# Kernel optimization log

Measured on AMD Instinct MI355X. Metric: run time of the kernel, lower is better.

Reference implementation:

```python
import jax, jax.numpy as jnp
import numpy as np

T, B, E, H = 2048, 4, 1024, 16
D = E // H  # head_dim = 64
SCALING = D ** -0.5


def setup_inputs() -> dict:
    key = jax.random.key(0)
    ks = jax.random.split(key, 5)
    w_scale = (2.0 / (E + E)) ** 0.5  # xavier_uniform-ish std
    return {
        "query": jax.random.normal(ks[0], (T, B, E), dtype=jnp.float32),
        "q_weight": jax.random.normal(ks[1], (E, E), dtype=jnp.float32) * w_scale,
        "k_weight": jax.random.normal(ks[2], (E, E), dtype=jnp.float32) * w_scale,
        "v_weight": jax.random.normal(ks[3], (E, E), dtype=jnp.float32) * w_scale,
        "out_proj_weight": jax.random.normal(ks[4], (E, E), dtype=jnp.float32) * w_scale,
        "q_bias": jnp.zeros((E,), dtype=jnp.float32),
        "k_bias": jnp.zeros((E,), dtype=jnp.float32),
        "v_bias": jnp.zeros((E,), dtype=jnp.float32),
        "out_proj_bias": jnp.zeros((E,), dtype=jnp.float32),
    }


def reference(query, q_weight, k_weight, v_weight, out_proj_weight,
              q_bias, k_bias, v_bias, out_proj_bias):
    # Linear projections: y = x @ W.T + b  (torch F.linear convention)
    q = jnp.einsum('tbe,fe->tbf', query, q_weight) + q_bias
    k = jnp.einsum('tbe,fe->tbf', query, k_weight) + k_bias
    v = jnp.einsum('tbe,fe->tbf', query, v_weight) + v_bias
    # split heads: [T, B, H, D]
    q = q.reshape(T, B, H, D) * SCALING
    k = k.reshape(T, B, H, D)
    v = v.reshape(T, B, H, D)
    # attention scores [B, H, T, T] over keys s
    scores = jnp.einsum('tbhd,sbhd->bhts', q, k)
    attn = jax.nn.softmax(scores, axis=-1)
    # context [T, B, H, D] -> [T, B, E]
    ctx = jnp.einsum('bhts,sbhd->tbhd', attn, v).reshape(T, B, E)
    # output projection
    out = jnp.einsum('tbe,fe->tbf', ctx, out_proj_weight) + out_proj_bias
    return out
```

## Files before the change

kernel.cpp:

```cpp
#include <hip/hip_runtime.h>
#include <hip/hip_bf16.h>
#include <stdint.h>

#define T_   2048
#define B_   4
#define E_   1024
#define H_   16
#define D_   64
#define M_   8192
#define KDIM 1024

using bf16 = __hip_bfloat16;
typedef __attribute__((ext_vector_type(8)))  short bf16x8;
typedef __attribute__((ext_vector_type(4)))  float f32x4;
typedef __attribute__((ext_vector_type(16))) float f32x16;

#define QK_SCALE 0.180336880f

#if __has_builtin(__builtin_amdgcn_exp2f)
#define EXP2F(x) __builtin_amdgcn_exp2f(x)
#else
#define EXP2F(x) exp2f(x)
#endif

__device__ __forceinline__ void gload_lds16(const void* g, void* l) {
  __builtin_amdgcn_global_load_lds(
      (const __attribute__((address_space(1))) void*)g,
      (__attribute__((address_space(3))) void*)l, 16, 0, 0);
}

__device__ __forceinline__ uint32_t pack_bf16(float lo, float hi) {
  union { __hip_bfloat162 h2; uint32_t u; } cv;
  cv.h2 = __float22bfloat162_rn(float2{lo, hi});
  return cv.u;
}

__device__ __forceinline__ void plswap(uint32_t& a, uint32_t& b) {
#if __has_builtin(__builtin_amdgcn_permlane32_swap)
  typedef __attribute__((ext_vector_type(2))) unsigned int u32x2_t;
  u32x2_t r = __builtin_amdgcn_permlane32_swap(a, b, false, false);
  a = r[0]; b = r[1];
#else
  asm volatile("v_permlane32_swap_b32 %0, %1" : "+v"(a), "+v"(b));
#endif
}
__device__ __forceinline__ float comb_add32(float x) {
  union { float f; uint32_t u; } a, b; a.f = x; b.f = x;
  plswap(a.u, b.u);
  return a.f + b.f;
}

__global__ void k_cvt_all(const float* __restrict__ X,
                          const float* __restrict__ Wq, const float* __restrict__ Wk,
                          const float* __restrict__ Wv, const float* __restrict__ Wo,
                          bf16* __restrict__ Xb,
                          bf16* __restrict__ Wqb, bf16* __restrict__ Wkb,
                          bf16* __restrict__ Wvb, bf16* __restrict__ Wob) {
  int id = blockIdx.x;
  const float* src; bf16* dst; int base;
  if (id < 8192) { src = X; dst = Xb; base = id; }
  else {
    int w = (id - 8192) >> 10;
    base = (id - 8192) & 1023;
    src = (w == 0) ? Wq : (w == 1) ? Wk : (w == 2) ? Wv : Wo;
    dst = (w == 0) ? Wqb : (w == 1) ? Wkb : (w == 2) ? Wvb : Wob;
  }
  int i = base * 256 + threadIdx.x;
  float4 v = reinterpret_cast<const float4*>(src)[i];
  bf16* d = dst + (size_t)i * 4;
  d[0] = __float2bfloat16(v.x);
  d[1] = __float2bfloat16(v.y);
  d[2] = __float2bfloat16(v.z);
  d[3] = __float2bfloat16(v.w);
}

__device__ __forceinline__ void gemm_tile_body(
    const bf16* __restrict__ A, const bf16* __restrict__ Bw,
    int bm, int bn, bf16* sA, bf16* sB, f32x4 (&acc)[4][4])
{
  const int t    = threadIdx.x;
  const int wave = t >> 6;
  const int lane = t & 63;
  const int l15  = lane & 15, l4 = lane >> 4;
  const int wr = wave >> 1, wc = wave & 1;
  const int srow = t >> 3;
  const int sg   = t & 7;

  for (int k0 = 0; k0 < KDIM; k0 += 64) {
#pragma unroll
    for (int rd = 0; rd < 4; ++rd) {
      int row = rd * 32 + srow;
      const bf16* src = A + (size_t)(bm * 128 + row) * KDIM + k0 + ((sg ^ (row & 7)) * 8);
      gload_lds16(src, sA + rd * 2048 + wave * 512);
    }
#pragma unroll
    for (int rd = 0; rd < 4; ++rd) {
      int row = rd * 32 + srow;
      const bf16* src = Bw + (size_t)(bn * 128 + row) * KDIM + k0 + ((sg ^ (row & 7)) * 8);
      gload_lds16(src, sB + rd * 2048 + wave * 512);
    }
    __syncthreads();

#pragma unroll
    for (int kk = 0; kk < 2; ++kk) {
      bf16x8 af[4], bfr[4];
#pragma unroll
      for (int m = 0; m < 4; ++m) {
        int row = wr * 64 + m * 16 + l15;
        int ch  = (l4 + kk * 4) ^ (row & 7);
        af[m] = *(const bf16x8*)(sA + row * 64 + ch * 8);
      }
#pragma unroll
      for (int n = 0; n < 4; ++n) {
        int row = wc * 64 + n * 16 + l15;
        int ch  = (l4 + kk * 4) ^ (row & 7);
        bfr[n] = *(const bf16x8*)(sB + row * 64 + ch * 8);
      }
#pragma unroll
      for (int m = 0; m < 4; ++m)
#pragma unroll
        for (int n = 0; n < 4; ++n)
          acc[m][n] = __builtin_amdgcn_mfma_f32_16x16x32_bf16(af[m], bfr[n], acc[m][n], 0, 0, 0);
    }
    __syncthreads();
  }
}

__global__ __launch_bounds__(256, 2) void k_gemm_qkv(
    const bf16* __restrict__ A,
    const bf16* __restrict__ Wq, const bf16* __restrict__ Wk, const bf16* __restrict__ Wv,
    const float* __restrict__ bq, const float* __restrict__ bk, const float* __restrict__ bv,
    bf16* __restrict__ outQ)
{
  __shared__ bf16 sA[128 * 64];
  __shared__ bf16 sB[128 * 64];
  const int bid = blockIdx.x;
  const int swz = (bid & 7) * 192 + (bid >> 3);
  const int bm = swz & 63;
  const int bn = swz >> 6;
  const int which = bn >> 3;
  const int bnn = bn & 7;
  const bf16* Bw = (which == 0) ? Wq : (which == 1) ? Wk : Wv;
  const float* bias = (which == 0) ? bq : (which == 1) ? bk : bv;
  const float scale = (which == 0) ? QK_SCALE : 1.0f;
  bf16* outb = outQ + (size_t)which * M_ * E_;

  f32x4 acc[4][4] = {};
  gemm_tile_body(A, Bw, bm, bnn, sA, sB, acc);

  const int lane = threadIdx.x & 63;
  const int l15 = lane & 15, l4 = lane >> 4;
  const int wave = threadIdx.x >> 6;
  const int wr = wave >> 1, wc = wave & 1;
#pragma unroll
  for (int m = 0; m < 4; ++m) {
#pragma unroll
    for (int n = 0; n < 4; ++n) {
      int gc = bnn * 128 + wc * 64 + n * 16 + l15;
      float bv_ = bias[gc];
#pragma unroll
      for (int r = 0; r < 4; ++r) {
        int gr = bm * 128 + wr * 64 + m * 16 + l4 * 4 + r;
        float v = (acc[m][n][r] + bv_) * scale;
        int tt = gr >> 2, bb = gr & 3;
        int hh = gc >> 6, dd = gc & 63;
        outb[(((size_t)(bb * H_ + hh)) * T_ + tt) * D_ + dd] = __float2bfloat16(v);
      }
    }
  }
}

__global__ __launch_bounds__(256, 2) void k_gemm_out(
    const bf16* __restrict__ A, const bf16* __restrict__ Bw,
    const float* __restrict__ bias, float* __restrict__ outf)
{
  __shared__ bf16 sA[128 * 64];
  __shared__ bf16 sB[128 * 64];
  const int bid = blockIdx.x;
  const int swz = (bid & 7) * 64 + (bid >> 3);
  const int bm = swz & 63;
  const int bn = swz >> 6;

  f32x4 acc[4][4] = {};
  gemm_tile_body(A, Bw, bm, bn, sA, sB, acc);

  const int lane = threadIdx.x & 63;
  const int l15 = lane & 15, l4 = lane >> 4;
  const int wave = threadIdx.x >> 6;
  const int wr = wave >> 1, wc = wave & 1;
#pragma unroll
  for (int m = 0; m < 4; ++m) {
#pragma unroll
    for (int n = 0; n < 4; ++n) {
      int gc = bn * 128 + wc * 64 + n * 16 + l15;
      float bv_ = bias[gc];
#pragma unroll
      for (int r = 0; r < 4; ++r) {
        int gr = bm * 128 + wr * 64 + m * 16 + l4 * 4 + r;
        outf[(size_t)gr * E_ + gc] = acc[m][n][r] + bv_;
      }
    }
  }
}

__global__ __launch_bounds__(256, 4) void k_attn3(
    const bf16* __restrict__ Qb, const bf16* __restrict__ Kb,
    const bf16* __restrict__ Vb, bf16* __restrict__ ctx)
{
  __shared__ bf16 sK [64 * 64];
  __shared__ bf16 sVT[64 * 64];

  const int t    = threadIdx.x;
  const int wave = t >> 6;
  const int lane = t & 63;
  const int l31  = lane & 31;
  const int h    = lane >> 5;

  const int bid = blockIdx.x;
  const int swz = (bid & 7) * 128 + (bid >> 3);
  const int bh  = swz >> 4;
  const int qt  = swz & 15;
  const int q0  = qt * 128;
  const size_t headoff = (size_t)bh * T_ * D_;

  const int qrow = q0 + wave * 32 + l31;
  bf16x8 qf[4];
#pragma unroll
  for (int kc = 0; kc < 4; ++kc)
    qf[kc] = *(const bf16x8*)(Qb + headoff + (size_t)qrow * 64 + kc * 16 + 8 * h);

  f32x16 acc0 = {}, acc1 = {};
  float lrun = 0.f;

  const int srow = t >> 3, sg = t & 7;
  const int vkey = (t >> 3) * 2, vd0 = (t & 7) * 8;

  for (int kt = 0; kt < T_ / 64; ++kt) {
    const bf16* ktile = Kb + headoff + (size_t)(kt * 64) * D_;
#pragma unroll
    for (int rd = 0; rd < 2; ++rd) {
      int row = rd * 32 + srow;
      gload_lds16(ktile + (size_t)row * 64 + ((sg ^ (row & 7)) * 8),
                  sK + rd * 2048 + wave * 512);
    }
    const bf16* vtile = Vb + headoff + (size_t)(kt * 64) * D_;
    bf16x8 va = *(const bf16x8*)(vtile + (size_t)vkey * 64 + vd0);
    bf16x8 vb = *(const bf16x8*)(vtile + (size_t)(vkey + 1) * 64 + vd0);
#pragma unroll
    for (int j = 0; j < 8; ++j) {
      int d = vd0 + j;
      int slot = (vkey >> 3) ^ (d & 7) ^ (d >> 3);
      uint32_t pk = (uint32_t)(uint16_t)va[j] | ((uint32_t)(uint16_t)vb[j] << 16);
      *reinterpret_cast<uint32_t*>(sVT + d * 64 + slot * 8 + (vkey & 7)) = pk;
    }
    __syncthreads();

    f32x16 s0 = {}, s1 = {};
    __builtin_amdgcn_s_setprio(1);
#pragma unroll
    for (int kc = 0; kc < 4; ++kc) {
      int slot = ((2 * kc + h) ^ (l31 & 7)) * 8;
      bf16x8 a0 = *(const bf16x8*)(sK + l31 * 64 + slot);
      bf16x8 a1 = *(const bf16x8*)(sK + (32 + l31) * 64 + slot);
      s0 = __builtin_amdgcn_mfma_f32_32x32x16_bf16(a0, qf[kc], s0, 0, 0, 0);
      s1 = __builtin_amdgcn_mfma_f32_32x32x16_bf16(a1, qf[kc], s1, 0, 0, 0);
    }
    __builtin_amdgcn_s_setprio(0);

    float psum = 0.f;
#pragma unroll
    for (int r = 0; r < 16; ++r) { s0[r] = EXP2F(s0[r]); psum += s0[r]; }
#pragma unroll
    for (int r = 0; r < 16; ++r) { s1[r] = EXP2F(s1[r]); psum += s1[r]; }
    lrun += psum;

    uint32_t u[8][2];
#pragma unroll
    for (int g = 0; g < 4; ++g) {
      u[g][0]     = pack_bf16(s0[g * 4 + 0], s0[g * 4 + 1]);
      u[g][1]     = pack_bf16(s0[g * 4 + 2], s0[g * 4 + 3]);
      u[4 + g][0] = pack_bf16(s1[g * 4 + 0], s1[g * 4 + 1]);
      u[4 + g][1] = pack_bf16(s1[g * 4 + 2], s1[g * 4 + 3]);
    }

    bf16x8 pa[4];
#pragma unroll
    for (int ks = 0; ks < 4; ++ks) {
      uint32_t w0 = u[2 * ks][0], w2 = u[2 * ks + 1][0];
      uint32_t w1 = u[2 * ks][1], w3 = u[2 * ks + 1][1];
      plswap(w0, w2);
      plswap(w1, w3);
      union { uint32_t w[4]; bf16x8 v; } cv;
      cv.w[0] = w0; cv.w[1] = w1; cv.w[2] = w2; cv.w[3] = w3;
      pa[ks] = cv.v;
    }

    __builtin_amdgcn_s_setprio(1);
#pragma unroll
    for (int ks = 0; ks < 4; ++ks) {
      int d0 = l31, d1 = 32 + l31;
      bf16x8 v0 = *(const bf16x8*)(sVT + d0 * 64 + (((2 * ks + h) ^ (d0 & 7) ^ (d0 >> 3)) * 8));
      bf16x8 v1 = *(const bf16x8*)(sVT + d1 * 64 + (((2 * ks + h) ^ (d1 & 7) ^ (d1 >> 3)) * 8));
      acc0 = __builtin_amdgcn_mfma_f32_32x32x16_bf16(v0, pa[ks], acc0, 0, 0, 0);
      acc1 = __builtin_amdgcn_mfma_f32_32x32x16_bf16(v1, pa[ks], acc1, 0, 0, 0);
    }
    __builtin_amdgcn_s_setprio(0);
    __syncthreads();
  }

  float lt = comb_add32(lrun);
  float rinv = 1.0f / lt;
  const int b = bh >> 4, hh = bh & 15;
#pragma unroll
  for (int dt = 0; dt < 2; ++dt) {
#pragma unroll
    for (int g = 0; g < 4; ++g) {
      float e0 = (dt ? acc1[g * 4 + 0] : acc0[g * 4 + 0]) * rinv;
      float e1 = (dt ? acc1[g * 4 + 1] : acc0[g * 4 + 1]) * rinv;
      float e2 = (dt ? acc1[g * 4 + 2] : acc0[g * 4 + 2]) * rinv;
      float e3 = (dt ? acc1[g * 4 + 3] : acc0[g * 4 + 3]) * rinv;
      int dbase = dt * 32 + g * 8 + 4 * h;
      uint2 wv = { pack_bf16(e0, e1), pack_bf16(e2, e3) };
      *reinterpret_cast<uint2*>(ctx + ((size_t)qrow * B_ + b) * E_ + hh * 64 + dbase) = wv;
    }
  }
}

extern "C" void kernel_launch(void* const* d_in, const int* in_sizes, int n_in,
                              void* d_out, int out_size, void* d_ws, size_t ws_size,
                              hipStream_t stream) {
  const float* X  = (const float*)d_in[0];
  const float* Wq = (const float*)d_in[1];
  const float* Wk = (const float*)d_in[2];
  const float* Wv = (const float*)d_in[3];
  const float* Wo = (const float*)d_in[4];
  const float* bq = (const float*)d_in[5];
  const float* bk = (const float*)d_in[6];
  const float* bv = (const float*)d_in[7];
  const float* bo = (const float*)d_in[8];
  float* out = (float*)d_out;

  char* ws = (char*)d_ws;
  const size_t XB   = (size_t)M_ * E_ * 2;
  const size_t WB   = (size_t)E_ * E_ * 2;
  bf16* Xb  = (bf16*)(ws);
  bf16* Wqb = (bf16*)(ws + XB);
  bf16* Wkb = (bf16*)(ws + XB + WB);
  bf16* Wvb = (bf16*)(ws + XB + 2 * WB);
  bf16* Wob = (bf16*)(ws + XB + 3 * WB);
  bf16* Qb  = (bf16*)(ws + XB + 4 * WB);
  bf16* Kb  = (bf16*)(ws + 2 * XB + 4 * WB);
  bf16* Vb  = (bf16*)(ws + 3 * XB + 4 * WB);
  bf16* Cx  = Xb;

  k_cvt_all<<<12288, 256, 0, stream>>>(X, Wq, Wk, Wv, Wo, Xb, Wqb, Wkb, Wvb, Wob);

  k_gemm_qkv<<<1536, 256, 0, stream>>>(Xb, Wqb, Wkb, Wvb, bq, bk, bv, Qb);

  k_attn3<<<1024, 256, 0, stream>>>(Qb, Kb, Vb, Cx);

  k_gemm_out<<<512, 256, 0, stream>>>(Cx, Wob, bo, out);
}
```

Baseline: 196.0 us.

## Double-buffer K/V tiles in attention and raise GEMM occupancy bounds

The attention kernel now keeps two LDS buffers each for K and transposed V. It prefetches the next K tile (async global-to-LDS) and the next V registers while the current tile is computed, which removes the trailing per-iteration barrier. The aim is to hide global-load latency behind the QK and PV MFMA work. Separately, both GEMM kernels raise their launch-bounds occupancy hint from 2 to 3 blocks, which caps registers per thread and may cause spills. LDS use per attention block doubles to 32KB.

```diff
diff --git a/kernel.cpp b/kernel.cpp
--- a/kernel.cpp
+++ b/kernel.cpp
@@ -126,7 +126,7 @@
   }
 }
 
-__global__ __launch_bounds__(256, 2) void k_gemm_qkv(
+__global__ __launch_bounds__(256, 3) void k_gemm_qkv(
     const bf16* __restrict__ A,
     const bf16* __restrict__ Wq, const bf16* __restrict__ Wk, const bf16* __restrict__ Wv,
     const float* __restrict__ bq, const float* __restrict__ bk, const float* __restrict__ bv,
@@ -170,7 +170,7 @@
   }
 }
 
-__global__ __launch_bounds__(256, 2) void k_gemm_out(
+__global__ __launch_bounds__(256, 3) void k_gemm_out(
     const bf16* __restrict__ A, const bf16* __restrict__ Bw,
     const float* __restrict__ bias, float* __restrict__ outf)
 {
@@ -203,12 +203,12 @@
   }
 }
 
-__global__ __launch_bounds__(256, 4) void k_attn3(
+__global__ __launch_bounds__(256, 4) void k_attn4(
     const bf16* __restrict__ Qb, const bf16* __restrict__ Kb,
     const bf16* __restrict__ Vb, bf16* __restrict__ ctx)
 {
-  __shared__ bf16 sK [64 * 64];
-  __shared__ bf16 sVT[64 * 64];
+  __shared__ bf16 sKbuf [2 * 64 * 64];
+  __shared__ bf16 sVTbuf[2 * 64 * 64];
 
   const int t    = threadIdx.x;
   const int wave = t >> 6;
@@ -235,17 +235,20 @@
   const int srow = t >> 3, sg = t & 7;
   const int vkey = (t >> 3) * 2, vd0 = (t & 7) * 8;
 
+#pragma unroll
+  for (int rd = 0; rd < 2; ++rd) {
+    int row = rd * 32 + srow;
+    gload_lds16(Kb + headoff + (size_t)row * 64 + ((sg ^ (row & 7)) * 8),
+                sKbuf + rd * 2048 + wave * 512);
+  }
+  bf16x8 va = *(const bf16x8*)(Vb + headoff + (size_t)vkey * 64 + vd0);
+  bf16x8 vb = *(const bf16x8*)(Vb + headoff + (size_t)(vkey + 1) * 64 + vd0);
+
   for (int kt = 0; kt < T_ / 64; ++kt) {
-    const bf16* ktile = Kb + headoff + (size_t)(kt * 64) * D_;
-#pragma unroll
-    for (int rd = 0; rd < 2; ++rd) {
-      int row = rd * 32 + srow;
-      gload_lds16(ktile + (size_t)row * 64 + ((sg ^ (row & 7)) * 8),
-                  sK + rd * 2048 + wave * 512);
-    }
-    const bf16* vtile = Vb + headoff + (size_t)(kt * 64) * D_;
-    bf16x8 va = *(const bf16x8*)(vtile + (size_t)vkey * 64 + vd0);
-    bf16x8 vb = *(const bf16x8*)(vtile + (size_t)(vkey + 1) * 64 + vd0);
+    const int cur = kt & 1;
+    bf16* sK  = sKbuf  + cur * 4096;
+    bf16* sVT = sVTbuf + cur * 4096;
+
 #pragma unroll
     for (int j = 0; j < 8; ++j) {
       int d = vd0 + j;
@@ -254,6 +257,20 @@
       *reinterpret_cast<uint32_t*>(sVT + d * 64 + slot * 8 + (vkey & 7)) = pk;
     }
     __syncthreads();
+
+    if (kt < T_ / 64 - 1) {
+      bf16* sKn = sKbuf + (1 - cur) * 4096;
+      const bf16* ktile = Kb + headoff + (size_t)((kt + 1) * 64) * D_;
+#pragma unroll
+      for (int rd = 0; rd < 2; ++rd) {
+        int row = rd * 32 + srow;
+        gload_lds16(ktile + (size_t)row * 64 + ((sg ^ (row & 7)) * 8),
+                    sKn + rd * 2048 + wave * 512);
+      }
+      const bf16* vtile = Vb + headoff + (size_t)((kt + 1) * 64) * D_;
+      va = *(const bf16x8*)(vtile + (size_t)vkey * 64 + vd0);
+      vb = *(const bf16x8*)(vtile + (size_t)(vkey + 1) * 64 + vd0);
+    }
 
     f32x16 s0 = {}, s1 = {};
     __builtin_amdgcn_s_setprio(1);
@@ -305,7 +322,6 @@
       acc1 = __builtin_amdgcn_mfma_f32_32x32x16_bf16(v1, pa[ks], acc1, 0, 0, 0);
     }
     __builtin_amdgcn_s_setprio(0);
-    __syncthreads();
   }
 
   float lt = comb_add32(lrun);
@@ -357,7 +373,7 @@
 
   k_gemm_qkv<<<1536, 256, 0, stream>>>(Xb, Wqb, Wkb, Wvb, bq, bk, bv, Qb);
 
-  k_attn3<<<1024, 256, 0, stream>>>(Qb, Kb, Vb, Cx);
+  k_attn4<<<1024, 256, 0, stream>>>(Qb, Kb, Vb, Cx);
 
   k_gemm_out<<<512, 256, 0, stream>>>(Cx, Wob, bo, out);
 }
```

Measured after the change: 204.2 us. +4.2%, slower.
